# Kernel optimization log

Measured on AMD Instinct MI355X. Metric: run time of the kernel, lower is better.

Reference implementation:

```python
import jax, jax.numpy as jnp
import numpy as np

GRID_SIZE = 48   # -> 97x97 in-plane grid
Z_DEPTH = 1
EPS = 1e-8


def plane_vw(n):
    # Plane basis from normal: R = R0 + s*V + t*W
    n = n / jnp.linalg.norm(n)
    nx, ny, nz = n[0], n[1], n[2]
    beta = 1.0 / jnp.sqrt(1.0 - nz * nz)
    v = jnp.stack([-ny * beta, nx * beta, jnp.zeros_like(beta)])
    w = jnp.stack([-nz * v[1], nz * v[0], 1.0 / beta])
    return n, v, w


def make_grids():
    gxy = np.arange(-GRID_SIZE, GRID_SIZE + 1, dtype=np.float32)
    gz = np.arange(Z_DEPTH, dtype=np.float32)
    v, w, _ = np.meshgrid(gxy, gxy, gz, indexing='xy')  # (G,G,Z)
    r = np.sqrt(v[..., -1] ** 2 + w[..., -1] ** 2)       # (G,G)
    phi = np.arctan2(w[..., -1], v[..., -1])             # (G,G)
    return jnp.asarray(v), jnp.asarray(w), jnp.asarray(phi)


def trilinear_sample(vol, grid):
    # vol: (C,D,H,W); grid: (Do,Ho,Wo,3) normalized (x,y,z) in [-1,1]
    # F.grid_sample semantics: trilinear, zero padding, align_corners=False
    C, D, H, W = vol.shape
    ix = ((grid[..., 0] + 1.0) * W - 1.0) * 0.5
    iy = ((grid[..., 1] + 1.0) * H - 1.0) * 0.5
    iz = ((grid[..., 2] + 1.0) * D - 1.0) * 0.5
    x0 = jnp.floor(ix); y0 = jnp.floor(iy); z0 = jnp.floor(iz)
    wx = ix - x0; wy = iy - y0; wz = iz - z0
    x0i = x0.astype(jnp.int32); y0i = y0.astype(jnp.int32); z0i = z0.astype(jnp.int32)
    out = jnp.zeros((C,) + grid.shape[:-1], dtype=vol.dtype)
    for dz, wgt_z in ((0, 1.0 - wz), (1, wz)):
        for dy, wgt_y in ((0, 1.0 - wy), (1, wy)):
            for dx, wgt_x in ((0, 1.0 - wx), (1, wx)):
                xc = x0i + dx; yc = y0i + dy; zc = z0i + dz
                valid = ((xc >= 0) & (xc < W) & (yc >= 0) & (yc < H)
                         & (zc >= 0) & (zc < D))
                xs = jnp.clip(xc, 0, W - 1)
                ys = jnp.clip(yc, 0, H - 1)
                zs = jnp.clip(zc, 0, D - 1)
                val = vol[:, zs, ys, xs]            # (C,Do,Ho,Wo) gather
                wgt = (wgt_z * wgt_y * wgt_x) * valid.astype(vol.dtype)
                out = out + val * wgt[None]
    return out


def grad_edge2(f, axis):
    # torch.gradient(spacing=1, edge_order=2) along one axis
    f = jnp.moveaxis(f, axis, -1)
    interior = (f[..., 2:] - f[..., :-2]) * 0.5
    first = -1.5 * f[..., 0:1] + 2.0 * f[..., 1:2] - 0.5 * f[..., 2:3]
    last = 1.5 * f[..., -1:] - 2.0 * f[..., -2:-1] + 0.5 * f[..., -3:-2]
    g = jnp.concatenate([first, interior, last], axis=-1)
    return jnp.moveaxis(g, -1, axis)


def forward(f, plane_normal, origin):
    if f.ndim == 4:
        f = f[None]
    n, pv, pw = plane_vw(plane_normal)
    v, w, phi = make_grids()                      # v,w: (G,G,Z)
    # plane grid: (Z,G,G,3) = v*V + w*W + origin
    grid = (jnp.moveaxis(v, -1, 0)[..., None] * pv
            + jnp.moveaxis(w, -1, 0)[..., None] * pw
            + origin)
    D, H, W = f.shape[-3:]
    whd = jnp.array([W, H, D], dtype=f.dtype)
    gnorm = grid * (2.0 / (whd - 1.0 + EPS)) - 1.0
    f_p = trilinear_sample(f[0], gnorm)[None]     # (1,C,Z,G,G)
    vwn = jnp.stack([pv, pw, n], axis=0)          # (3,3)
    f_p = jnp.einsum('bcdhw,nc->bndhw', f_p, vwn)
    # polar basis matrix (n=3, h, w, c=3)
    s, c = jnp.sin(phi), jnp.cos(phi)
    z = jnp.zeros_like(c); o = jnp.ones_like(c)
    P = jnp.stack([jnp.stack([c, s, z], -1),
                   jnp.stack([-s, c, z], -1),
                   jnp.stack([z, z, o], -1)], 0)
    f_pol = jnp.einsum('bcdhw,nhwc->bndhw', f_p, P)
    gy = grad_edge2(f_pol, -2)
    gx = grad_edge2(f_pol, -1)
    gz = jnp.zeros_like(gx)
    grads = jnp.stack([gx, gy, gz], axis=1)       # (b,3,c,d,h,w)
    grads_axial = jnp.einsum('bcidhw,nhwc->bnidhw', grads, P)
    return f_p, grads_axial


def setup_inputs() -> dict:
    key = jax.random.key(0)
    f = jax.random.normal(key, (1, 3, 150, 512, 512), dtype=jnp.float32)
    plane_normal = jnp.array([1.0, 1.0, 0.25], dtype=jnp.float32)
    origin = jnp.array([256.0, 256.0, 75.0], dtype=jnp.float32)
    return {'f': f, 'plane_normal': plane_normal, 'origin': origin}


def reference(f, plane_normal, origin):
    return forward(f, plane_normal, origin)
```

## Files before the change

kernel.cpp:

```cpp
#include <hip/hip_runtime.h>

#define GSZ   97
#define NPTS  (GSZ * GSZ)
#define DVOL  150
#define HVOL  512
#define WVOL  512
#define TILE  16
#define HALO  2
#define SPAN  (TILE + 2 * HALO)
#define NTILE ((GSZ + TILE - 1) / TILE)

struct Basis {
    float pvx, pvy, pvz;
    float pwx, pwy, pwz;
    float nx,  ny,  nz;
    float ox,  oy,  oz;
};

__device__ inline void fpol_at(const float* __restrict__ f, int h, int w,
                               const Basis& B, float* __restrict__ fpol,
                               float* __restrict__ fproj)
{
    const float gv = (float)(w - 48);
    const float gw = (float)(h - 48);

    const float px = gv * B.pvx + gw * B.pwx + B.ox;
    const float py = gv * B.pvy + gw * B.pwy + B.oy;
    const float pz = gv * B.pvz + gw * B.pwz + B.oz;

    const float EPSF = 1e-8f;
    const float gnx = px * (2.0f / ((float)WVOL - 1.0f + EPSF)) - 1.0f;
    const float gny = py * (2.0f / ((float)HVOL - 1.0f + EPSF)) - 1.0f;
    const float gnz = pz * (2.0f / ((float)DVOL - 1.0f + EPSF)) - 1.0f;
    const float ix = ((gnx + 1.0f) * (float)WVOL - 1.0f) * 0.5f;
    const float iy = ((gny + 1.0f) * (float)HVOL - 1.0f) * 0.5f;
    const float iz = ((gnz + 1.0f) * (float)DVOL - 1.0f) * 0.5f;

    const float x0f = floorf(ix), y0f = floorf(iy), z0f = floorf(iz);
    const float wx = ix - x0f, wy = iy - y0f, wz = iz - z0f;
    const int x0 = (int)x0f, y0 = (int)y0f, z0 = (int)z0f;

    const size_t cstride = (size_t)DVOL * HVOL * WVOL;

    float acc0 = 0.0f, acc1 = 0.0f, acc2 = 0.0f;
#pragma unroll
    for (int dz = 0; dz < 2; ++dz) {
        const float wgz = dz ? wz : 1.0f - wz;
        const int zc = z0 + dz;
        const bool vz = (zc >= 0) && (zc < DVOL);
        const int zs = min(max(zc, 0), DVOL - 1);
#pragma unroll
        for (int dy = 0; dy < 2; ++dy) {
            const float wgy = dy ? wy : 1.0f - wy;
            const int yc = y0 + dy;
            const bool vy = (yc >= 0) && (yc < HVOL);
            const int ys = min(max(yc, 0), HVOL - 1);
#pragma unroll
            for (int dx = 0; dx < 2; ++dx) {
                const float wgx = dx ? wx : 1.0f - wx;
                const int xc = x0 + dx;
                const bool vx = (xc >= 0) && (xc < WVOL);
                const int xs = min(max(xc, 0), WVOL - 1);
                const float wgt =
                    wgz * wgy * wgx * ((vz && vy && vx) ? 1.0f : 0.0f);
                const size_t base = ((size_t)zs * HVOL + ys) * (size_t)WVOL + xs;
                acc0 += f[base] * wgt;
                acc1 += f[base + cstride] * wgt;
                acc2 += f[base + 2 * cstride] * wgt;
            }
        }
    }

    const float p0 = acc0 * B.pvx + acc1 * B.pvy + acc2 * B.pvz;
    const float p1 = acc0 * B.pwx + acc1 * B.pwy + acc2 * B.pwz;
    const float p2 = acc0 * B.nx  + acc1 * B.ny  + acc2 * B.nz;
    fproj[0] = p0; fproj[1] = p1; fproj[2] = p2;

    const float r = sqrtf(gv * gv + gw * gw);
    const float s = (r > 0.0f) ? gw / r : 0.0f;
    const float c = (r > 0.0f) ? gv / r : 1.0f;
    fpol[0] =  c * p0 + s * p1;
    fpol[1] = -s * p0 + c * p1;
    fpol[2] =  p2;
}

__global__ __launch_bounds__(512)
void planar_tile_kernel(const float* __restrict__ f,
                        const float* __restrict__ pn,
                        const float* __restrict__ org,
                        float* __restrict__ out)
{
    __shared__ float spol[SPAN][SPAN][3];

    const int r0 = blockIdx.y * TILE;
    const int c0 = blockIdx.x * TILE;
    const int tid = threadIdx.x;

    Basis B;
    {
        float n0 = pn[0], n1 = pn[1], n2 = pn[2];
        const float nrm = sqrtf(n0 * n0 + n1 * n1 + n2 * n2);
        n0 /= nrm; n1 /= nrm; n2 /= nrm;
        const float beta = 1.0f / sqrtf(1.0f - n2 * n2);
        B.pvx = -n1 * beta; B.pvy = n0 * beta; B.pvz = 0.0f;
        B.pwx = -n2 * B.pvy; B.pwy = n2 * B.pvx; B.pwz = 1.0f / beta;
        B.nx = n0; B.ny = n1; B.nz = n2;
        B.ox = org[0]; B.oy = org[1]; B.oz = org[2];
    }

    for (int e = tid; e < SPAN * SPAN; e += (int)blockDim.x) {
        const int sr = e / SPAN;
        const int sc = e - sr * SPAN;
        const int gh = r0 - HALO + sr;
        const int gw = c0 - HALO + sc;
        if (gh >= 0 && gh < GSZ && gw >= 0 && gw < GSZ) {
            float fpol[3], fproj[3];
            fpol_at(f, gh, gw, B, fpol, fproj);
            spol[sr][sc][0] = fpol[0];
            spol[sr][sc][1] = fpol[1];
            spol[sr][sc][2] = fpol[2];
            if (gh >= r0 && gh < r0 + TILE && gw >= c0 && gw < c0 + TILE) {
                const int idx = gh * GSZ + gw;
                out[0 * NPTS + idx] = fproj[0];
                out[1 * NPTS + idx] = fproj[1];
                out[2 * NPTS + idx] = fproj[2];
            }
        }
    }

    __syncthreads();

    if (tid >= TILE * TILE) return;
    const int lr = tid >> 4;
    const int lc = tid & 15;
    const int h = r0 + lr;
    const int w = c0 + lc;
    if (h >= GSZ || w >= GSZ) return;

    const int sr = lr + HALO;
    const int sc = lc + HALO;

    float gxv[3], gyv[3];

    if (w == 0) {
#pragma unroll
        for (int i = 0; i < 3; ++i)
            gxv[i] = -1.5f * spol[sr][2][i] + 2.0f * spol[sr][3][i]
                     - 0.5f * spol[sr][4][i];
    } else if (w == GSZ - 1) {
        const int b = (GSZ - 1) - c0 + HALO;
#pragma unroll
        for (int i = 0; i < 3; ++i)
            gxv[i] = 1.5f * spol[sr][b][i] - 2.0f * spol[sr][b - 1][i]
                     + 0.5f * spol[sr][b - 2][i];
    } else {
#pragma unroll
        for (int i = 0; i < 3; ++i)
            gxv[i] = 0.5f * (spol[sr][sc + 1][i] - spol[sr][sc - 1][i]);
    }

    if (h == 0) {
#pragma unroll
        for (int i = 0; i < 3; ++i)
            gyv[i] = -1.5f * spol[2][sc][i] + 2.0f * spol[3][sc][i]
                     - 0.5f * spol[4][sc][i];
    } else if (h == GSZ - 1) {
        const int b = (GSZ - 1) - r0 + HALO;
#pragma unroll
        for (int i = 0; i < 3; ++i)
            gyv[i] = 1.5f * spol[b][sc][i] - 2.0f * spol[b - 1][sc][i]
                     + 0.5f * spol[b - 2][sc][i];
    } else {
#pragma unroll
        for (int i = 0; i < 3; ++i)
            gyv[i] = 0.5f * (spol[sr + 1][sc][i] - spol[sr - 1][sc][i]);
    }

    const float gv = (float)(w - 48);
    const float gw = (float)(h - 48);
    const float r = sqrtf(gv * gv + gw * gw);
    const float s = (r > 0.0f) ? gw / r : 0.0f;
    const float c = (r > 0.0f) ? gv / r : 1.0f;

    const int idx = h * GSZ + w;
    float* __restrict__ o2 = out + 3 * NPTS;
#pragma unroll
    for (int i = 0; i < 3; ++i) {
        o2[(0 * 3 + i) * NPTS + idx] =  c * gxv[i] + s * gyv[i];
        o2[(1 * 3 + i) * NPTS + idx] = -s * gxv[i] + c * gyv[i];
        o2[(2 * 3 + i) * NPTS + idx] = 0.0f;
    }
}

extern "C" void kernel_launch(void* const* d_in, const int* in_sizes, int n_in,
                              void* d_out, int out_size, void* d_ws, size_t ws_size,
                              hipStream_t stream) {
    const float* f   = (const float*)d_in[0];
    const float* pn  = (const float*)d_in[1];
    const float* org = (const float*)d_in[2];
    float* out = (float*)d_out;

    dim3 grid(NTILE, NTILE);
    planar_tile_kernel<<<grid, 512, 0, stream>>>(f, pn, org, out);
}
```

Before: 11.09 us.

## Stage per-tile volume bounding box in LDS before trilinear sampling

Each block computes the axis-aligned bounding box of volume voxels its 20x20 sample tile touches. If the box fits in 20x20x23 per channel, it cooperatively loads the box into shared memory and the trilinear gathers read from LDS instead of scattered global loads. Otherwise it falls back to direct global gathers. This adds a large block-wide preload (about 27.6K floats) that may fetch more voxels than the 8 corners per point actually need.

```diff
diff --git a/kernel.cpp b/kernel.cpp
--- a/kernel.cpp
+++ b/kernel.cpp
@@ -10,6 +10,10 @@
 #define SPAN  (TILE + 2 * HALO)
 #define NTILE ((GSZ + TILE - 1) / TILE)
 
+#define SX 20
+#define SY 20
+#define SZ 23
+
 struct Basis {
     float pvx, pvy, pvz;
     float pwx, pwy, pwz;
@@ -17,79 +21,13 @@
     float ox,  oy,  oz;
 };
 
-__device__ inline void fpol_at(const float* __restrict__ f, int h, int w,
-                               const Basis& B, float* __restrict__ fpol,
-                               float* __restrict__ fproj)
-{
-    const float gv = (float)(w - 48);
-    const float gw = (float)(h - 48);
-
-    const float px = gv * B.pvx + gw * B.pwx + B.ox;
-    const float py = gv * B.pvy + gw * B.pwy + B.oy;
-    const float pz = gv * B.pvz + gw * B.pwz + B.oz;
-
-    const float EPSF = 1e-8f;
-    const float gnx = px * (2.0f / ((float)WVOL - 1.0f + EPSF)) - 1.0f;
-    const float gny = py * (2.0f / ((float)HVOL - 1.0f + EPSF)) - 1.0f;
-    const float gnz = pz * (2.0f / ((float)DVOL - 1.0f + EPSF)) - 1.0f;
-    const float ix = ((gnx + 1.0f) * (float)WVOL - 1.0f) * 0.5f;
-    const float iy = ((gny + 1.0f) * (float)HVOL - 1.0f) * 0.5f;
-    const float iz = ((gnz + 1.0f) * (float)DVOL - 1.0f) * 0.5f;
-
-    const float x0f = floorf(ix), y0f = floorf(iy), z0f = floorf(iz);
-    const float wx = ix - x0f, wy = iy - y0f, wz = iz - z0f;
-    const int x0 = (int)x0f, y0 = (int)y0f, z0 = (int)z0f;
-
-    const size_t cstride = (size_t)DVOL * HVOL * WVOL;
-
-    float acc0 = 0.0f, acc1 = 0.0f, acc2 = 0.0f;
-#pragma unroll
-    for (int dz = 0; dz < 2; ++dz) {
-        const float wgz = dz ? wz : 1.0f - wz;
-        const int zc = z0 + dz;
-        const bool vz = (zc >= 0) && (zc < DVOL);
-        const int zs = min(max(zc, 0), DVOL - 1);
-#pragma unroll
-        for (int dy = 0; dy < 2; ++dy) {
-            const float wgy = dy ? wy : 1.0f - wy;
-            const int yc = y0 + dy;
-            const bool vy = (yc >= 0) && (yc < HVOL);
-            const int ys = min(max(yc, 0), HVOL - 1);
-#pragma unroll
-            for (int dx = 0; dx < 2; ++dx) {
-                const float wgx = dx ? wx : 1.0f - wx;
-                const int xc = x0 + dx;
-                const bool vx = (xc >= 0) && (xc < WVOL);
-                const int xs = min(max(xc, 0), WVOL - 1);
-                const float wgt =
-                    wgz * wgy * wgx * ((vz && vy && vx) ? 1.0f : 0.0f);
-                const size_t base = ((size_t)zs * HVOL + ys) * (size_t)WVOL + xs;
-                acc0 += f[base] * wgt;
-                acc1 += f[base + cstride] * wgt;
-                acc2 += f[base + 2 * cstride] * wgt;
-            }
-        }
-    }
-
-    const float p0 = acc0 * B.pvx + acc1 * B.pvy + acc2 * B.pvz;
-    const float p1 = acc0 * B.pwx + acc1 * B.pwy + acc2 * B.pwz;
-    const float p2 = acc0 * B.nx  + acc1 * B.ny  + acc2 * B.nz;
-    fproj[0] = p0; fproj[1] = p1; fproj[2] = p2;
-
-    const float r = sqrtf(gv * gv + gw * gw);
-    const float s = (r > 0.0f) ? gw / r : 0.0f;
-    const float c = (r > 0.0f) ? gv / r : 1.0f;
-    fpol[0] =  c * p0 + s * p1;
-    fpol[1] = -s * p0 + c * p1;
-    fpol[2] =  p2;
-}
-
 __global__ __launch_bounds__(512)
 void planar_tile_kernel(const float* __restrict__ f,
                         const float* __restrict__ pn,
                         const float* __restrict__ org,
                         float* __restrict__ out)
 {
+    __shared__ float sbox[3][SZ][SY][SX];
     __shared__ float spol[SPAN][SPAN][3];
 
     const int r0 = blockIdx.y * TILE;
@@ -108,23 +46,145 @@
         B.ox = org[0]; B.oy = org[1]; B.oz = org[2];
     }
 
-    for (int e = tid; e < SPAN * SPAN; e += (int)blockDim.x) {
+    const float EPSF = 1e-8f;
+    const float xsc = (float)WVOL / ((float)WVOL - 1.0f + EPSF);
+    const float ysc = (float)HVOL / ((float)HVOL - 1.0f + EPSF);
+    const float zsc = (float)DVOL / ((float)DVOL - 1.0f + EPSF);
+
+    const float gvlo = (float)(c0 - HALO - 48);
+    const float gvhi = (float)(c0 + TILE + HALO - 1 - 48);
+    const float gwlo = (float)(r0 - HALO - 48);
+    const float gwhi = (float)(r0 + TILE + HALO - 1 - 48);
+
+    int xmin, ymin, zmin, sx, sy, sz;
+    {
+        const float avx = B.pvx * xsc, awx = B.pwx * xsc, bx = B.ox * xsc - 0.5f;
+        const float avy = B.pvy * ysc, awy = B.pwy * ysc, by = B.oy * ysc - 0.5f;
+        const float avz = B.pvz * zsc, awz = B.pwz * zsc, bz = B.oz * zsc - 0.5f;
+
+        float x00 = gvlo * avx + gwlo * awx + bx, x01 = gvlo * avx + gwhi * awx + bx;
+        float x10 = gvhi * avx + gwlo * awx + bx, x11 = gvhi * avx + gwhi * awx + bx;
+        float y00 = gvlo * avy + gwlo * awy + by, y01 = gvlo * avy + gwhi * awy + by;
+        float y10 = gvhi * avy + gwlo * awy + by, y11 = gvhi * avy + gwhi * awy + by;
+        float z00 = gvlo * avz + gwlo * awz + bz, z01 = gvlo * avz + gwhi * awz + bz;
+        float z10 = gvhi * avz + gwlo * awz + bz, z11 = gvhi * avz + gwhi * awz + bz;
+
+        const float M = 0.01f;
+        const float ixmin = fminf(fminf(x00, x01), fminf(x10, x11)) - M;
+        const float ixmax = fmaxf(fmaxf(x00, x01), fmaxf(x10, x11)) + M;
+        const float iymin = fminf(fminf(y00, y01), fminf(y10, y11)) - M;
+        const float iymax = fmaxf(fmaxf(y00, y01), fmaxf(y10, y11)) + M;
+        const float izmin = fminf(fminf(z00, z01), fminf(z10, z11)) - M;
+        const float izmax = fmaxf(fmaxf(z00, z01), fmaxf(z10, z11)) + M;
+
+        xmin = min(max((int)floorf(ixmin), 0), WVOL - 1);
+        ymin = min(max((int)floorf(iymin), 0), HVOL - 1);
+        zmin = min(max((int)floorf(izmin), 0), DVOL - 1);
+        const int xmax = min(max((int)floorf(ixmax) + 1, 0), WVOL - 1);
+        const int ymax = min(max((int)floorf(iymax) + 1, 0), HVOL - 1);
+        const int zmax = min(max((int)floorf(izmax) + 1, 0), DVOL - 1);
+        sx = xmax - xmin + 1; sy = ymax - ymin + 1; sz = zmax - zmin + 1;
+    }
+    const bool useLds = (sx <= SX) && (sy <= SY) && (sz <= SZ);
+
+    const int cstride = DVOL * HVOL * WVOL;
+
+    if (useLds) {
+        for (int i = tid; i < 3 * SZ * SY * SX; i += 512) {
+            const int lx = i % SX;
+            int t = i / SX;
+            const int ly = t % SY;
+            t /= SY;
+            const int lz = t % SZ;
+            const int ch = t / SZ;
+            const int gx = min(xmin + lx, WVOL - 1);
+            const int gy = min(ymin + ly, HVOL - 1);
+            const int gz = min(zmin + lz, DVOL - 1);
+            sbox[ch][lz][ly][lx] = f[ch * cstride + (gz * HVOL + gy) * WVOL + gx];
+        }
+        __syncthreads();
+    }
+
+    for (int e = tid; e < SPAN * SPAN; e += 512) {
         const int sr = e / SPAN;
         const int sc = e - sr * SPAN;
         const int gh = r0 - HALO + sr;
-        const int gw = c0 - HALO + sc;
-        if (gh >= 0 && gh < GSZ && gw >= 0 && gw < GSZ) {
-            float fpol[3], fproj[3];
-            fpol_at(f, gh, gw, B, fpol, fproj);
-            spol[sr][sc][0] = fpol[0];
-            spol[sr][sc][1] = fpol[1];
-            spol[sr][sc][2] = fpol[2];
-            if (gh >= r0 && gh < r0 + TILE && gw >= c0 && gw < c0 + TILE) {
-                const int idx = gh * GSZ + gw;
-                out[0 * NPTS + idx] = fproj[0];
-                out[1 * NPTS + idx] = fproj[1];
-                out[2 * NPTS + idx] = fproj[2];
+        const int gwc = c0 - HALO + sc;
+        if (gh < 0 || gh >= GSZ || gwc < 0 || gwc >= GSZ) continue;
+
+        const float gv = (float)(gwc - 48);
+        const float gw = (float)(gh - 48);
+
+        const float px = gv * B.pvx + gw * B.pwx + B.ox;
+        const float py = gv * B.pvy + gw * B.pwy + B.oy;
+        const float pz = gv * B.pvz + gw * B.pwz + B.oz;
+        const float gnx = px * (2.0f / ((float)WVOL - 1.0f + EPSF)) - 1.0f;
+        const float gny = py * (2.0f / ((float)HVOL - 1.0f + EPSF)) - 1.0f;
+        const float gnz = pz * (2.0f / ((float)DVOL - 1.0f + EPSF)) - 1.0f;
+        const float ix = ((gnx + 1.0f) * (float)WVOL - 1.0f) * 0.5f;
+        const float iy = ((gny + 1.0f) * (float)HVOL - 1.0f) * 0.5f;
+        const float iz = ((gnz + 1.0f) * (float)DVOL - 1.0f) * 0.5f;
+
+        const float x0f = floorf(ix), y0f = floorf(iy), z0f = floorf(iz);
+        const float wx = ix - x0f, wy = iy - y0f, wz = iz - z0f;
+        const int x0 = (int)x0f, y0 = (int)y0f, z0 = (int)z0f;
+
+        float acc0 = 0.0f, acc1 = 0.0f, acc2 = 0.0f;
+#pragma unroll
+        for (int dz = 0; dz < 2; ++dz) {
+            const float wgz = dz ? wz : 1.0f - wz;
+            const int zc = z0 + dz;
+            const bool vz = (zc >= 0) && (zc < DVOL);
+            const int zs = min(max(zc, 0), DVOL - 1);
+#pragma unroll
+            for (int dy = 0; dy < 2; ++dy) {
+                const float wgy = dy ? wy : 1.0f - wy;
+                const int yc = y0 + dy;
+                const bool vy = (yc >= 0) && (yc < HVOL);
+                const int ys = min(max(yc, 0), HVOL - 1);
+#pragma unroll
+                for (int dx = 0; dx < 2; ++dx) {
+                    const float wgx = dx ? wx : 1.0f - wx;
+                    const int xc = x0 + dx;
+                    const bool vx = (xc >= 0) && (xc < WVOL);
+                    const int xs = min(max(xc, 0), WVOL - 1);
+                    const float wgt =
+                        wgz * wgy * wgx * ((vz && vy && vx) ? 1.0f : 0.0f);
+                    float v0, v1, v2;
+                    if (useLds) {
+                        const int lx = xs - xmin, lyy = ys - ymin, lzz = zs - zmin;
+                        v0 = sbox[0][lzz][lyy][lx];
+                        v1 = sbox[1][lzz][lyy][lx];
+                        v2 = sbox[2][lzz][lyy][lx];
+                    } else {
+                        const int base = (zs * HVOL + ys) * WVOL + xs;
+                        v0 = f[base];
+                        v1 = f[base + cstride];
+                        v2 = f[base + 2 * cstride];
+                    }
+                    acc0 += v0 * wgt;
+                    acc1 += v1 * wgt;
+                    acc2 += v2 * wgt;
+                }
             }
+        }
+
+        const float p0 = acc0 * B.pvx + acc1 * B.pvy + acc2 * B.pvz;
+        const float p1 = acc0 * B.pwx + acc1 * B.pwy + acc2 * B.pwz;
+        const float p2 = acc0 * B.nx  + acc1 * B.ny  + acc2 * B.nz;
+
+        const float r = sqrtf(gv * gv + gw * gw);
+        const float s = (r > 0.0f) ? gw / r : 0.0f;
+        const float c = (r > 0.0f) ? gv / r : 1.0f;
+        spol[sr][sc][0] =  c * p0 + s * p1;
+        spol[sr][sc][1] = -s * p0 + c * p1;
+        spol[sr][sc][2] =  p2;
+
+        if (gh >= r0 && gh < r0 + TILE && gwc >= c0 && gwc < c0 + TILE) {
+            const int idx = gh * GSZ + gwc;
+            out[0 * NPTS + idx] = p0;
+            out[1 * NPTS + idx] = p1;
+            out[2 * NPTS + idx] = p2;
         }
     }
 
```

New measurement: 20.14 us. 81.5% more time.
